# Kernel tuning notes

Measured on AMD Instinct MI355X. Metric: run time of the kernel, lower is better.

Reference implementation:

```python
import jax, jax.numpy as jnp
import numpy as np
from jax import lax

B, C, H, W = 16, 256, 32, 32
DH = 32
HEADS = C // DH          # 8
WSZ = 4                  # window size
K = 4                    # top-k windows
MR = 4                   # mlp_ratio
NWIN = (H // WSZ) * (W // WSZ)  # 64
WS = WSZ * WSZ                  # 16 tokens per window
EPS = 1e-5


def setup_inputs() -> dict:
    key = jax.random.key(0)
    ks = jax.random.split(key, 8)
    w = lambda i, shape: jax.random.normal(ks[i], shape, jnp.float32) * 0.02
    d = {
        'x': jax.random.normal(ks[0], (B, C, H, W), jnp.float32),
        'bn0_g': jax.random.uniform(ks[1], (C,), jnp.float32, 0.5, 1.5),
        'bn0_b': jnp.zeros((C,), jnp.float32),
        'bn0_m': jnp.zeros((C,), jnp.float32),
        'bn0_v': jnp.ones((C,), jnp.float32),
        'w_qkv': w(2, (3 * C, C)),
        'w_merge': w(3, (C, C)),
        'b_merge': jnp.zeros((C,), jnp.float32),
        'w1': w(4, (MR * C, C)),
        'bn1_g': jax.random.uniform(ks[5], (MR * C,), jnp.float32, 0.5, 1.5),
        'bn1_b': jnp.zeros((MR * C,), jnp.float32),
        'bn1_m': jnp.zeros((MR * C,), jnp.float32),
        'bn1_v': jnp.ones((MR * C,), jnp.float32),
        'dw': w(6, (MR * C, 1, 3, 3)),
        'bn2_g': jax.random.uniform(ks[7], (MR * C,), jnp.float32, 0.5, 1.5),
        'bn2_b': jnp.zeros((MR * C,), jnp.float32),
        'bn2_m': jnp.zeros((MR * C,), jnp.float32),
        'bn2_v': jnp.ones((MR * C,), jnp.float32),
        'w2': w(0, (C, MR * C)),
        'bn3_g': jax.random.uniform(ks[1], (C,), jnp.float32, 0.5, 1.5),
        'bn3_b': jnp.zeros((C,), jnp.float32),
        'bn3_m': jnp.zeros((C,), jnp.float32),
        'bn3_v': jnp.ones((C,), jnp.float32),
    }
    return d


def _bn(x, g, b, m, v):
    # eval-mode BatchNorm2d on NCHW
    s = (g / jnp.sqrt(v + EPS))
    return (x - m[None, :, None, None]) * s[None, :, None, None] + b[None, :, None, None]


def _win(t):
    # [B, C, H, W] -> [B, HEADS, NWIN, WS, DH]
    nh, nw = H // WSZ, W // WSZ
    t = t.reshape(B, HEADS, DH, nh, WSZ, nw, WSZ)
    return t.transpose(0, 1, 3, 5, 4, 6, 2).reshape(B, HEADS, NWIN, WS, DH)


def _unwin(t):
    # [B, HEADS, NWIN, WS, DH] -> [B, C, H, W]
    nh, nw = H // WSZ, W // WSZ
    t = t.reshape(B, HEADS, nh, nw, WSZ, WSZ, DH)
    return t.transpose(0, 1, 6, 2, 4, 3, 5).reshape(B, C, H, W)


def _forward(x, bn0_g, bn0_b, bn0_m, bn0_v, w_qkv, w_merge, b_merge,
             w1, bn1_g, bn1_b, bn1_m, bn1_v, dw, bn2_g, bn2_b, bn2_m, bn2_v,
             w2, bn3_g, bn3_b, bn3_m, bn3_v):
    # qkv projection: BN -> GELU -> 1x1 conv (no bias)
    h = jax.nn.gelu(_bn(x, bn0_g, bn0_b, bn0_m, bn0_v), approximate=False)
    qkv = jnp.einsum('oc,bchw->bohw', w_qkv, h)
    q, k, v = jnp.split(qkv, 3, axis=1)

    qw, kw, vw = _win(q), _win(k), _win(v)  # [B,H,NWIN,WS,DH]
    scale = 1.0 / jnp.sqrt(jnp.float32(DH))

    # window-level descriptors -> window-window affinity -> top-k selection
    wsc = jnp.einsum('bhid,bhjd->bhij', qw.mean(3), kw.mean(3)) * scale
    idx = lax.top_k(wsc, K)[1]  # [B,H,NWIN,K]

    # gather top-k kv windows per query window (irregular access)
    gather = jax.vmap(jax.vmap(lambda t, ix: t[ix]))  # over B, HEADS
    kk = gather(kw, idx).reshape(B, HEADS, NWIN, K * WS, DH)
    vv = gather(vw, idx).reshape(B, HEADS, NWIN, K * WS, DH)

    attn = jax.nn.softmax(jnp.einsum('bhnqd,bhnkd->bhnqk', qw, kk) * scale, axis=-1)
    msg = jnp.einsum('bhnqk,bhnkd->bhnqd', attn, vv)
    msg = _unwin(msg)

    # merge (1x1 conv with bias) + residual
    x = x + jnp.einsum('oc,bchw->bohw', w_merge, msg) + b_merge[None, :, None, None]

    # MB mlp: 1x1 expand -> BN -> GELU -> depthwise 3x3 -> BN -> GELU -> 1x1 -> BN
    h = jnp.einsum('oc,bchw->bohw', w1, x)
    h = jax.nn.gelu(_bn(h, bn1_g, bn1_b, bn1_m, bn1_v), approximate=False)
    h = lax.conv_general_dilated(h, dw, (1, 1), 'SAME',
                                 feature_group_count=MR * C,
                                 dimension_numbers=('NCHW', 'OIHW', 'NCHW'))
    h = jax.nn.gelu(_bn(h, bn2_g, bn2_b, bn2_m, bn2_v), approximate=False)
    h = jnp.einsum('oc,bchw->bohw', w2, h)
    h = _bn(h, bn3_g, bn3_b, bn3_m, bn3_v)
    return x + h


def reference(x, bn0_g, bn0_b, bn0_m, bn0_v, w_qkv, w_merge, b_merge,
              w1, bn1_g, bn1_b, bn1_m, bn1_v, dw, bn2_g, bn2_b, bn2_m, bn2_v,
              w2, bn3_g, bn3_b, bn3_m, bn3_v):
    return _forward(x, bn0_g, bn0_b, bn0_m, bn0_v, w_qkv, w_merge, b_merge,
                    w1, bn1_g, bn1_b, bn1_m, bn1_v, dw, bn2_g, bn2_b, bn2_m, bn2_v,
                    w2, bn3_g, bn3_b, bn3_m, bn3_v)
```

## Files before the change

### kernel.cpp

```cpp
#include <hip/hip_runtime.h>
#include <hip/hip_bf16.h>

#define EPSV 1e-5f

typedef short bf16x8 __attribute__((ext_vector_type(8)));
typedef float f32x4 __attribute__((ext_vector_type(4)));

__device__ __forceinline__ float gelu_f(float x) {
    return 0.5f * x * (1.0f + erff(x * 0.70710678118654752f));
}
__device__ __forceinline__ float b2f(unsigned short u) {
    union { float f; unsigned i; } c; c.i = ((unsigned)u) << 16; return c.f;
}
__device__ __forceinline__ unsigned short f2b(float f) {
    __hip_bfloat16 h = __float2bfloat16(f);
    return *reinterpret_cast<unsigned short*>(&h);
}
__device__ __forceinline__ float lo16f(unsigned v) {
    union { float f; unsigned i; } c; c.i = v << 16; return c.f;
}
__device__ __forceinline__ float hi16f(unsigned v) {
    union { float f; unsigned i; } c; c.i = v & 0xffff0000u; return c.f;
}
__device__ __forceinline__ void gload16(const unsigned short* g, unsigned short* l) {
    __builtin_amdgcn_global_load_lds(
        (const __attribute__((address_space(1))) void*)g,
        (__attribute__((address_space(3))) void*)l, 16, 0, 0);
}

__global__ __launch_bounds__(256) void wcvt_k(const float* __restrict__ w,
                                              unsigned short* __restrict__ o, int n4) {
    int i = blockIdx.x * 256 + threadIdx.x;
    if (i >= n4) return;
    float4 v = ((const float4*)w)[i];
    ushort4 u = make_ushort4(f2b(v.x), f2b(v.y), f2b(v.z), f2b(v.w));
    ((ushort4*)o)[i] = u;
}

__global__ __launch_bounds__(256) void wprep_k(const float* __restrict__ wdw,
    const float* __restrict__ g, const float* __restrict__ bt,
    const float* __restrict__ mu, const float* __restrict__ va,
    float* __restrict__ wt, float* __restrict__ scf, float* __restrict__ shf) {
    int ch = blockIdx.x * 256 + threadIdx.x;
    #pragma unroll
    for (int tap = 0; tap < 9; ++tap)
        wt[tap * 1024 + ch] = wdw[ch * 9 + tap];
    float s = g[ch] * rsqrtf(va[ch] + EPSV);
    scf[ch] = s;
    shf[ch] = bt[ch] - mu[ch] * s;
}

__global__ __launch_bounds__(256) void bn0tr_k(const float* __restrict__ x,
    const float* __restrict__ g, const float* __restrict__ bt,
    const float* __restrict__ mu, const float* __restrict__ va,
    unsigned short* __restrict__ h0b, float* __restrict__ xt) {
    __shared__ float tile[64][65];
    int hw0 = blockIdx.x * 64, c0 = blockIdx.y * 64, b = blockIdx.z;
    int t = threadIdx.x;
    int cl = t >> 6, hl = t & 63;
    #pragma unroll
    for (int r = 0; r < 16; ++r)
        tile[r * 4 + cl][hl] = x[((size_t)(b * 256 + c0 + r * 4 + cl)) * 1024 + hw0 + hl];
    __syncthreads();
    int c = c0 + (t & 63);
    float s = g[c] * rsqrtf(va[c] + EPSV);
    float m_ = mu[c], be = bt[c];
    #pragma unroll
    for (int r = 0; r < 16; ++r) {
        int hl2 = r * 4 + (t >> 6);
        float v = tile[t & 63][hl2];
        size_t o = ((size_t)(b * 1024 + hw0 + hl2)) * 256 + c;
        xt[o] = v;
        h0b[o] = f2b(gelu_f((v - m_) * s + be));
    }
}

__global__ __launch_bounds__(256) void hm_k(const float* __restrict__ xt,
    const float* __restrict__ g, const float* __restrict__ bt,
    const float* __restrict__ mu, const float* __restrict__ va,
    float* __restrict__ hm) {
    int blk = blockIdx.x;
    int b = blk >> 6, win = blk & 63;
    int c = threadIdx.x;
    int base = (win >> 3) * 128 + (win & 7) * 4;
    float s = g[c] * rsqrtf(va[c] + EPSV);
    float m_ = mu[c], be = bt[c];
    float acc = 0.f;
    #pragma unroll
    for (int ty = 0; ty < 4; ++ty)
        #pragma unroll
        for (int tx = 0; tx < 4; ++tx) {
            float v = xt[((size_t)(b * 1024 + base + ty * 32 + tx)) * 256 + c];
            acc += gelu_f((v - m_) * s + be);
        }
    hm[(size_t)blk * 256 + c] = acc * (1.f / 16.f);
}

template <int MODE>
__global__ __launch_bounds__(256) void mgemm(
    const unsigned short* __restrict__ A, const unsigned short* __restrict__ X,
    unsigned short* __restrict__ outb, float* __restrict__ outf,
    const float* __restrict__ res,
    const float* __restrict__ p0, const float* __restrict__ p1,
    const float* __restrict__ p2, const float* __restrict__ p3,
    int M, int Kd) {
    __shared__ __align__(16) unsigned short As[4096];
    __shared__ __align__(16) unsigned short Bs[4096];
    const int t = threadIdx.x;
    const int wid = t >> 6, lane = t & 63;
    const int n0 = blockIdx.x * 128, m0 = blockIdx.y * 128, b = blockIdx.z;
    const unsigned short* Ab = A + (size_t)m0 * Kd;
    const unsigned short* Xb = X + ((size_t)b * 1024 + n0) * Kd;

    const int srow = lane >> 2;
    const int skb  = (lane & 3) * 8;
    const int wr = wid >> 1, wc = wid & 1;
    const int lr = lane & 15;
    const int lk = (lane >> 4) * 8;

    f32x4 acc[4][4] = {};

    for (int k0 = 0; k0 < Kd; k0 += 32) {
        #pragma unroll
        for (int i = 0; i < 2; ++i) {
            int chunk = wid * 2 + i;
            int row = chunk * 16 + srow;
            gload16(Ab + (size_t)row * Kd + k0 + skb, &As[chunk * 512]);
            gload16(Xb + (size_t)row * Kd + k0 + skb, &Bs[chunk * 512]);
        }
        __syncthreads();
        bf16x8 af[4], bfv[4];
        #pragma unroll
        for (int mi = 0; mi < 4; ++mi)
            af[mi] = *(const bf16x8*)&As[(wr * 64 + mi * 16 + lr) * 32 + lk];
        #pragma unroll
        for (int ni = 0; ni < 4; ++ni)
            bfv[ni] = *(const bf16x8*)&Bs[(wc * 64 + ni * 16 + lr) * 32 + lk];
        #pragma unroll
        for (int mi = 0; mi < 4; ++mi)
            #pragma unroll
            for (int ni = 0; ni < 4; ++ni)
                acc[mi][ni] = __builtin_amdgcn_mfma_f32_16x16x32_bf16(
                    af[mi], bfv[ni], acc[mi][ni], 0, 0, 0);
        __syncthreads();
    }

    const int crow = (lane >> 4) * 4;
    #pragma unroll
    for (int ni = 0; ni < 4; ++ni) {
        const int n = n0 + wc * 64 + ni * 16 + lr;
        #pragma unroll
        for (int mi = 0; mi < 4; ++mi) {
            const int m = m0 + wr * 64 + mi * 16 + crow;
            f32x4 v = acc[mi][ni];
            size_t o = ((size_t)b * 1024 + n) * (size_t)M + m;
            if (MODE == 0) {
                *(ushort4*)(outb + o) = make_ushort4(f2b(v[0]), f2b(v[1]), f2b(v[2]), f2b(v[3]));
            } else if (MODE == 1) {
                float4 r = *(const float4*)(res + o);
                float4 bi = *(const float4*)(p0 + m);
                float w0 = v[0] + r.x + bi.x, w1 = v[1] + r.y + bi.y;
                float w2 = v[2] + r.z + bi.z, w3 = v[3] + r.w + bi.w;
                *(float4*)(outf + o) = make_float4(w0, w1, w2, w3);
                *(ushort4*)(outb + o) = make_ushort4(f2b(w0), f2b(w1), f2b(w2), f2b(w3));
            } else if (MODE == 2) {
                float4 gg = *(const float4*)(p0 + m);
                float4 be = *(const float4*)(p1 + m);
                float4 mm = *(const float4*)(p2 + m);
                float4 vv = *(const float4*)(p3 + m);
                float h0 = gelu_f((v[0] - mm.x) * (gg.x * rsqrtf(vv.x + EPSV)) + be.x);
                float h1 = gelu_f((v[1] - mm.y) * (gg.y * rsqrtf(vv.y + EPSV)) + be.y);
                float h2 = gelu_f((v[2] - mm.z) * (gg.z * rsqrtf(vv.z + EPSV)) + be.z);
                float h3 = gelu_f((v[3] - mm.w) * (gg.w * rsqrtf(vv.w + EPSV)) + be.w);
                *(ushort4*)(outb + o) = make_ushort4(f2b(h0), f2b(h1), f2b(h2), f2b(h3));
            } else {
                float4 gg = *(const float4*)(p0 + m);
                float4 be = *(const float4*)(p1 + m);
                float4 mm = *(const float4*)(p2 + m);
                float4 vv = *(const float4*)(p3 + m);
                float4 r = *(const float4*)(res + o);
                float y0 = (v[0] - mm.x) * (gg.x * rsqrtf(vv.x + EPSV)) + be.x + r.x;
                float y1 = (v[1] - mm.y) * (gg.y * rsqrtf(vv.y + EPSV)) + be.y + r.y;
                float y2 = (v[2] - mm.z) * (gg.z * rsqrtf(vv.z + EPSV)) + be.z + r.z;
                float y3 = (v[3] - mm.w) * (gg.w * rsqrtf(vv.w + EPSV)) + be.w + r.w;
                *(float4*)(outf + o) = make_float4(y0, y1, y2, y3);
            }
        }
    }
}

__global__ __launch_bounds__(256) void desc2_k(const float* __restrict__ hm,
                                               const float* __restrict__ w_qkv,
                                               float* __restrict__ qkd) {
    __shared__ float As[16][64];
    __shared__ float Bs[16][64];
    float acc[4][4] = {{0.f}};
    const int t = threadIdx.x;
    const int tn = t & 15, tm = t >> 4;
    const int n0 = blockIdx.x * 64;
    const int m0 = blockIdx.y * 64;
    for (int k0 = 0; k0 < 256; k0 += 16) {
        {
            int r  = t >> 2;
            int k4 = (t & 3) << 2;
            float4 a4 = *(const float4*)(w_qkv + (size_t)(m0 + r) * 256 + k0 + k4);
            As[k4 + 0][r] = a4.x; As[k4 + 1][r] = a4.y;
            As[k4 + 2][r] = a4.z; As[k4 + 3][r] = a4.w;
            float4 b4 = *(const float4*)(hm + (size_t)(n0 + r) * 256 + k0 + k4);
            Bs[k4 + 0][r] = b4.x; Bs[k4 + 1][r] = b4.y;
            Bs[k4 + 2][r] = b4.z; Bs[k4 + 3][r] = b4.w;
        }
        __syncthreads();
        #pragma unroll
        for (int kk = 0; kk < 16; ++kk) {
            float4 av = *(const float4*)&As[kk][tm << 2];
            float4 bv = *(const float4*)&Bs[kk][tn << 2];
            float a0[4] = {av.x, av.y, av.z, av.w};
            float b0[4] = {bv.x, bv.y, bv.z, bv.w};
            #pragma unroll
            for (int i = 0; i < 4; ++i)
                #pragma unroll
                for (int j = 0; j < 4; ++j)
                    acc[i][j] += a0[i] * b0[j];
        }
        __syncthreads();
    }
    #pragma unroll
    for (int j = 0; j < 4; ++j) {
        int row = n0 + (tn << 2) + j;
        float4 v = make_float4(acc[0][j], acc[1][j], acc[2][j], acc[3][j]);
        *(float4*)(qkd + (size_t)row * 512 + m0 + (tm << 2)) = v;
    }
}

__global__ __launch_bounds__(256) void aff_k(const float* __restrict__ qkd,
                                             int* __restrict__ idx_out) {
    int bh = blockIdx.x;
    int b = bh >> 3, h = bh & 7;
    __shared__ float qdl[64][33];
    __shared__ float kdl[64][33];
    __shared__ float wsc[64][65];
    int t = threadIdx.x;
    for (int e = t; e < 2048; e += 256) {
        int wn = e >> 5, d = e & 31;
        size_t src = ((size_t)(b * 64 + wn)) * 512 + h * 32 + d;
        qdl[wn][d] = qkd[src];
        kdl[wn][d] = qkd[src + 256];
    }
    __syncthreads();
    {
        int i = t >> 2, j0 = (t & 3) * 16;
        float s[16];
        #pragma unroll
        for (int j = 0; j < 16; ++j) s[j] = 0.f;
        #pragma unroll
        for (int d = 0; d < 32; ++d) {
            float qv = qdl[i][d];
            #pragma unroll
            for (int j = 0; j < 16; ++j) s[j] += qv * kdl[j0 + j][d];
        }
        #pragma unroll
        for (int j = 0; j < 16; ++j) wsc[i][j0 + j] = s[j];
    }
    __syncthreads();
    if (t < 64) {
        float bv[4] = {-1e30f, -1e30f, -1e30f, -1e30f};
        int   bi[4] = {0, 0, 0, 0};
        for (int j = 0; j < 64; ++j) {
            float v = wsc[t][j];
            if (v > bv[3]) {
                int p = 3;
                while (p > 0 && v > bv[p - 1]) {
                    bv[p] = bv[p - 1]; bi[p] = bi[p - 1]; --p;
                }
                bv[p] = v; bi[p] = j;
            }
        }
        int* o = idx_out + (bh * 64 + t) * 4;
        o[0] = bi[0]; o[1] = bi[1]; o[2] = bi[2]; o[3] = bi[3];
    }
}

__global__ __launch_bounds__(256) void attn_k(const unsigned short* __restrict__ qkv,
                                              const int* __restrict__ idx,
                                              unsigned short* __restrict__ msg) {
    int blk = blockIdx.x;
    int win = blk & 63;
    int bh = blk >> 6;
    int b = bh >> 3, h = bh & 7;
    __shared__ float qs[16][32];
    __shared__ float ks[64][32];
    __shared__ float vs[64][32];
    __shared__ float sc[16][64];
    __shared__ int widx[4];
    int t = threadIdx.x;
    if (t < 4) widx[t] = idx[(bh * 64 + win) * 4 + t];
    __syncthreads();
    int qb = (win >> 3) * 128 + (win & 7) * 4;
    for (int e = t; e < 512; e += 256) {
        int tok = e >> 5, d = e & 31;
        int hw = qb + (tok >> 2) * 32 + (tok & 3);
        qs[tok][d] = b2f(qkv[((size_t)(b * 1024 + hw)) * 768 + h * 32 + d]);
    }
    for (int e = t; e < 2048; e += 256) {
        int key = e >> 5, d = e & 31;
        int wsel = widx[key >> 4];
        int tok = key & 15;
        int hw = (wsel >> 3) * 128 + (wsel & 7) * 4 + (tok >> 2) * 32 + (tok & 3);
        size_t base = ((size_t)(b * 1024 + hw)) * 768 + h * 32 + d;
        ks[key][d] = b2f(qkv[base + 256]);
        vs[key][d] = b2f(qkv[base + 512]);
    }
    __syncthreads();
    const float scale = 0.17677669529663688f;
    for (int e = t; e < 1024; e += 256) {
        int r = e >> 6, cidx = e & 63;
        float s = 0.f;
        #pragma unroll
        for (int d = 0; d < 32; ++d) s += qs[r][d] * ks[cidx][d];
        sc[r][cidx] = s * scale;
    }
    __syncthreads();
    {
        int r = t >> 4, c0 = (t & 15) << 2;
        float v0 = sc[r][c0], v1 = sc[r][c0 + 1], v2 = sc[r][c0 + 2], v3 = sc[r][c0 + 3];
        float mx = fmaxf(fmaxf(v0, v1), fmaxf(v2, v3));
        #pragma unroll
        for (int m = 1; m < 16; m <<= 1) mx = fmaxf(mx, __shfl_xor(mx, m));
        float e0 = expf(v0 - mx), e1 = expf(v1 - mx), e2 = expf(v2 - mx), e3 = expf(v3 - mx);
        float sm = e0 + e1 + e2 + e3;
        #pragma unroll
        for (int m = 1; m < 16; m <<= 1) sm += __shfl_xor(sm, m);
        float inv = 1.0f / sm;
        sc[r][c0] = e0 * inv; sc[r][c0 + 1] = e1 * inv;
        sc[r][c0 + 2] = e2 * inv; sc[r][c0 + 3] = e3 * inv;
    }
    __syncthreads();
    for (int e = t; e < 512; e += 256) {
        int tok = e >> 5, d = e & 31;
        float s = 0.f;
        #pragma unroll
        for (int kk = 0; kk < 64; ++kk) s += sc[tok][kk] * vs[kk][d];
        int hw = qb + (tok >> 2) * 32 + (tok & 3);
        msg[((size_t)(b * 1024 + hw)) * 256 + h * 32 + d] = f2b(s);
    }
}

__global__ __launch_bounds__(256) void dw_k(const unsigned short* __restrict__ h1,
    const float* __restrict__ wt, const float* __restrict__ scf,
    const float* __restrict__ shf, unsigned short* __restrict__ h2) {
    int t = threadIdx.x;
    int c8 = t & 127;
    int pl = t >> 7;
    int blk = blockIdx.x;
    int b = blk >> 7;
    int rem = blk & 127;
    int y = rem >> 2;
    int x0 = (rem & 3) * 8;
    int ch0 = c8 * 8;

    float w[9][8];
    #pragma unroll
    for (int tap = 0; tap < 9; ++tap) {
        float4 a = *(const float4*)(wt + tap * 1024 + ch0);
        float4 bq = *(const float4*)(wt + tap * 1024 + ch0 + 4);
        w[tap][0] = a.x; w[tap][1] = a.y; w[tap][2] = a.z; w[tap][3] = a.w;
        w[tap][4] = bq.x; w[tap][5] = bq.y; w[tap][6] = bq.z; w[tap][7] = bq.w;
    }
    float sc[8], sh[8];
    {
        float4 a = *(const float4*)(scf + ch0);
        float4 bq = *(const float4*)(scf + ch0 + 4);
        sc[0]=a.x; sc[1]=a.y; sc[2]=a.z; sc[3]=a.w; sc[4]=bq.x; sc[5]=bq.y; sc[6]=bq.z; sc[7]=bq.w;
        float4 c = *(const float4*)(shf + ch0);
        float4 dq = *(const float4*)(shf + ch0 + 4);
        sh[0]=c.x; sh[1]=c.y; sh[2]=c.z; sh[3]=c.w; sh[4]=dq.x; sh[5]=dq.y; sh[6]=dq.z; sh[7]=dq.w;
    }

    const unsigned short* base = h1 + (size_t)b * 1048576;
    unsigned short* ob = h2 + (size_t)b * 1048576;

    #pragma unroll
    for (int j = 0; j < 4; ++j) {
        int x = x0 + pl + 2 * j;
        float acc[8] = {0.f,0.f,0.f,0.f,0.f,0.f,0.f,0.f};
        #pragma unroll
        for (int dy = -1; dy <= 1; ++dy) {
            int yy = y + dy;
            if (yy < 0 || yy > 31) continue;
            #pragma unroll
            for (int dx = -1; dx <= 1; ++dx) {
                int xx = x + dx;
                if (xx < 0 || xx > 31) continue;
                uint4 u = *(const uint4*)(base + (size_t)(yy * 32 + xx) * 1024 + ch0);
                int tap = (dy + 1) * 3 + (dx + 1);
                acc[0] += lo16f(u.x) * w[tap][0];
                acc[1] += hi16f(u.x) * w[tap][1];
                acc[2] += lo16f(u.y) * w[tap][2];
                acc[3] += hi16f(u.y) * w[tap][3];
                acc[4] += lo16f(u.z) * w[tap][4];
                acc[5] += hi16f(u.z) * w[tap][5];
                acc[6] += lo16f(u.w) * w[tap][6];
                acc[7] += hi16f(u.w) * w[tap][7];
            }
        }
        unsigned short r[8];
        #pragma unroll
        for (int c = 0; c < 8; ++c)
            r[c] = f2b(gelu_f(acc[c] * sc[c] + sh[c]));
        uint4 o;
        o.x = (unsigned)r[0] | ((unsigned)r[1] << 16);
        o.y = (unsigned)r[2] | ((unsigned)r[3] << 16);
        o.z = (unsigned)r[4] | ((unsigned)r[5] << 16);
        o.w = (unsigned)r[6] | ((unsigned)r[7] << 16);
        *(uint4*)(ob + (size_t)(y * 32 + x) * 1024 + ch0) = o;
    }
}

__global__ __launch_bounds__(256) void trout_k(const float* __restrict__ y,
                                               float* __restrict__ out) {
    __shared__ float tile[64][65];
    int hw0 = blockIdx.x * 64, c0 = blockIdx.y * 64, b = blockIdx.z;
    int t = threadIdx.x;
    #pragma unroll
    for (int r = 0; r < 16; ++r) {
        int hl = r * 4 + (t >> 6);
        tile[t & 63][hl] = y[((size_t)(b * 1024 + hw0 + hl)) * 256 + c0 + (t & 63)];
    }
    __syncthreads();
    #pragma unroll
    for (int r = 0; r < 16; ++r) {
        int cl = r * 4 + (t >> 6);
        out[((size_t)(b * 256 + c0 + cl)) * 1024 + hw0 + (t & 63)] = tile[cl][t & 63];
    }
}

extern "C" void kernel_launch(void* const* d_in, const int* in_sizes, int n_in,
                              void* d_out, int out_size, void* d_ws, size_t ws_size,
                              hipStream_t stream) {
    const float* x      = (const float*)d_in[0];
    const float* bn0_g  = (const float*)d_in[1];
    const float* bn0_b  = (const float*)d_in[2];
    const float* bn0_m  = (const float*)d_in[3];
    const float* bn0_v  = (const float*)d_in[4];
    const float* w_qkv  = (const float*)d_in[5];
    const float* w_merge= (const float*)d_in[6];
    const float* b_merge= (const float*)d_in[7];
    const float* w1     = (const float*)d_in[8];
    const float* bn1_g  = (const float*)d_in[9];
    const float* bn1_b  = (const float*)d_in[10];
    const float* bn1_m  = (const float*)d_in[11];
    const float* bn1_v  = (const float*)d_in[12];
    const float* dw     = (const float*)d_in[13];
    const float* bn2_g  = (const float*)d_in[14];
    const float* bn2_b  = (const float*)d_in[15];
    const float* bn2_m  = (const float*)d_in[16];
    const float* bn2_v  = (const float*)d_in[17];
    const float* w2     = (const float*)d_in[18];
    const float* bn3_g  = (const float*)d_in[19];
    const float* bn3_b  = (const float*)d_in[20];
    const float* bn3_m  = (const float*)d_in[21];
    const float* bn3_v  = (const float*)d_in[22];
    float* out = (float*)d_out;

    char* w = (char*)d_ws;
    unsigned short* h0b   = (unsigned short*)(w);
    unsigned short* qkvb  = (unsigned short*)(w + 8388608);
    unsigned short* msgb  = (unsigned short*)(w + 33554432);
    unsigned short* xrb   = (unsigned short*)(w + 41943040);
    unsigned short* h1b   = (unsigned short*)(w + 50331648);
    unsigned short* h2b   = (unsigned short*)(w + 83886080);
    float*  xt    = (float*)(w + 117440512);
    float*  xrf   = (float*)(w + 134217728);
    float*  yf    = (float*)(w + 150994944);
    float*  hm    = (float*)(w + 167772160);
    unsigned short* wqkvb = (unsigned short*)(w + 168820736);
    unsigned short* wmrgb = (unsigned short*)(w + 169213952);
    unsigned short* w1b   = (unsigned short*)(w + 169345024);
    unsigned short* w2b   = (unsigned short*)(w + 169869312);
    int*    idx   = (int*)(w + 170393600);
    float*  wtbuf = (float*)(w + 170524672);
    float*  scbuf = (float*)(w + 170561536);
    float*  shbuf = (float*)(w + 170565632);
    float*  qkdbuf= (float*)(w + 170569728);

    wcvt_k<<<192, 256, 0, stream>>>(w_qkv, wqkvb, 49152);
    wcvt_k<<<64,  256, 0, stream>>>(w_merge, wmrgb, 16384);
    wcvt_k<<<256, 256, 0, stream>>>(w1, w1b, 65536);
    wcvt_k<<<256, 256, 0, stream>>>(w2, w2b, 65536);
    wprep_k<<<4, 256, 0, stream>>>(dw, bn2_g, bn2_b, bn2_m, bn2_v, wtbuf, scbuf, shbuf);

    bn0tr_k<<<dim3(16, 4, 16), 256, 0, stream>>>(x, bn0_g, bn0_b, bn0_m, bn0_v, h0b, xt);
    hm_k<<<1024, 256, 0, stream>>>(xt, bn0_g, bn0_b, bn0_m, bn0_v, hm);
    mgemm<0><<<dim3(8, 6, 16), 256, 0, stream>>>(wqkvb, h0b, qkvb, nullptr,
        nullptr, nullptr, nullptr, nullptr, nullptr, 768, 256);
    desc2_k<<<dim3(16, 8), 256, 0, stream>>>(hm, w_qkv, qkdbuf);
    aff_k<<<128, 256, 0, stream>>>(qkdbuf, idx);
    attn_k<<<8192, 256, 0, stream>>>(qkvb, idx, msgb);
    mgemm<1><<<dim3(8, 2, 16), 256, 0, stream>>>(wmrgb, msgb, xrb, xrf,
        xt, b_merge, nullptr, nullptr, nullptr, 256, 256);
    mgemm<2><<<dim3(8, 8, 16), 256, 0, stream>>>(w1b, xrb, h1b, nullptr,
        nullptr, bn1_g, bn1_b, bn1_m, bn1_v, 1024, 256);
    dw_k<<<2048, 256, 0, stream>>>(h1b, wtbuf, scbuf, shbuf, h2b);
    mgemm<3><<<dim3(8, 2, 16), 256, 0, stream>>>(w2b, h2b, nullptr, yf,
        xrf, bn3_g, bn3_b, bn3_m, bn3_v, 256, 1024);
    trout_k<<<dim3(16, 4, 16), 256, 0, stream>>>(yf, out);
}
```

Measured before the change: 377.7 us.

## Rewrite windowed attention with per-wave MFMA tiles and bf16 shared memory

The attention kernel now handles one (batch, head, window) per wavefront, packing four into each block, and launches a quarter as many blocks. QK^T and PV are computed with 16x16x32 bf16 MFMA instructions instead of scalar fp32 dot products. Q, K and V are staged in shared memory as bf16 using vectorized 8-byte loads, with V stored transposed. Softmax runs directly on the MFMA accumulators. The aim is to remove the scalar-FMA and shared-memory bandwidth cost, at the price of rounding probabilities to bf16 and doing scattered 2-byte writes for the transposed V.

```diff
diff --git a/kernel.cpp b/kernel.cpp
--- a/kernel.cpp
+++ b/kernel.cpp
@@ -284,65 +284,92 @@
 __global__ __launch_bounds__(256) void attn_k(const unsigned short* __restrict__ qkv,
                                               const int* __restrict__ idx,
                                               unsigned short* __restrict__ msg) {
-    int blk = blockIdx.x;
-    int win = blk & 63;
-    int bh = blk >> 6;
-    int b = bh >> 3, h = bh & 7;
-    __shared__ float qs[16][32];
-    __shared__ float ks[64][32];
-    __shared__ float vs[64][32];
-    __shared__ float sc[16][64];
-    __shared__ int widx[4];
-    int t = threadIdx.x;
-    if (t < 4) widx[t] = idx[(bh * 64 + win) * 4 + t];
-    __syncthreads();
-    int qb = (win >> 3) * 128 + (win & 7) * 4;
-    for (int e = t; e < 512; e += 256) {
-        int tok = e >> 5, d = e & 31;
+    __shared__ __align__(16) unsigned short qs[4][16][40];
+    __shared__ __align__(16) unsigned short ks[4][64][40];
+    __shared__ __align__(16) unsigned short vt[4][32][72];
+    __shared__ __align__(16) unsigned short ps[4][16][72];
+    const int t = threadIdx.x;
+    const int wid = t >> 6, lane = t & 63;
+    const int g = blockIdx.x * 4 + wid;
+    const int win = g & 63;
+    const int bh = g >> 6;
+    const int b = bh >> 3, h = bh & 7;
+    const int qb = (win >> 3) * 128 + (win & 7) * 4;
+    const int* widx = idx + (bh * 64 + win) * 4;
+
+    for (int e = lane; e < 128; e += 64) {
+        int tok = e >> 3, d4 = (e & 7) * 4;
         int hw = qb + (tok >> 2) * 32 + (tok & 3);
-        qs[tok][d] = b2f(qkv[((size_t)(b * 1024 + hw)) * 768 + h * 32 + d]);
-    }
-    for (int e = t; e < 2048; e += 256) {
-        int key = e >> 5, d = e & 31;
+        uint2 u = *(const uint2*)&qkv[((size_t)(b * 1024 + hw)) * 768 + h * 32 + d4];
+        *(uint2*)&qs[wid][tok][d4] = u;
+    }
+    for (int e = lane; e < 512; e += 64) {
+        int key = e >> 3, d4 = (e & 7) * 4;
         int wsel = widx[key >> 4];
         int tok = key & 15;
         int hw = (wsel >> 3) * 128 + (wsel & 7) * 4 + (tok >> 2) * 32 + (tok & 3);
-        size_t base = ((size_t)(b * 1024 + hw)) * 768 + h * 32 + d;
-        ks[key][d] = b2f(qkv[base + 256]);
-        vs[key][d] = b2f(qkv[base + 512]);
+        size_t base = ((size_t)(b * 1024 + hw)) * 768 + h * 32 + d4;
+        uint2 uk = *(const uint2*)&qkv[base + 256];
+        uint2 uv = *(const uint2*)&qkv[base + 512];
+        *(uint2*)&ks[wid][key][d4] = uk;
+        vt[wid][d4 + 0][key] = (unsigned short)(uv.x & 0xffffu);
+        vt[wid][d4 + 1][key] = (unsigned short)(uv.x >> 16);
+        vt[wid][d4 + 2][key] = (unsigned short)(uv.y & 0xffffu);
+        vt[wid][d4 + 3][key] = (unsigned short)(uv.y >> 16);
     }
     __syncthreads();
+
+    const int lr = lane & 15;
+    const int lk8 = (lane >> 4) * 8;
     const float scale = 0.17677669529663688f;
-    for (int e = t; e < 1024; e += 256) {
-        int r = e >> 6, cidx = e & 63;
-        float s = 0.f;
-        #pragma unroll
-        for (int d = 0; d < 32; ++d) s += qs[r][d] * ks[cidx][d];
-        sc[r][cidx] = s * scale;
-    }
-    __syncthreads();
-    {
-        int r = t >> 4, c0 = (t & 15) << 2;
-        float v0 = sc[r][c0], v1 = sc[r][c0 + 1], v2 = sc[r][c0 + 2], v3 = sc[r][c0 + 3];
-        float mx = fmaxf(fmaxf(v0, v1), fmaxf(v2, v3));
+    f32x4 zero = {0.f, 0.f, 0.f, 0.f};
+
+    bf16x8 qA = *(const bf16x8*)&qs[wid][lr][lk8];
+    f32x4 sa[4];
+    #pragma unroll
+    for (int kt = 0; kt < 4; ++kt) {
+        bf16x8 kB = *(const bf16x8*)&ks[wid][kt * 16 + lr][lk8];
+        sa[kt] = __builtin_amdgcn_mfma_f32_16x16x32_bf16(qA, kB, zero, 0, 0, 0);
+    }
+    #pragma unroll
+    for (int i = 0; i < 4; ++i) {
+        float s0 = sa[0][i] * scale, s1 = sa[1][i] * scale;
+        float s2 = sa[2][i] * scale, s3 = sa[3][i] * scale;
+        float mx = fmaxf(fmaxf(s0, s1), fmaxf(s2, s3));
         #pragma unroll
         for (int m = 1; m < 16; m <<= 1) mx = fmaxf(mx, __shfl_xor(mx, m));
-        float e0 = expf(v0 - mx), e1 = expf(v1 - mx), e2 = expf(v2 - mx), e3 = expf(v3 - mx);
+        float e0 = expf(s0 - mx), e1 = expf(s1 - mx);
+        float e2 = expf(s2 - mx), e3 = expf(s3 - mx);
         float sm = e0 + e1 + e2 + e3;
         #pragma unroll
         for (int m = 1; m < 16; m <<= 1) sm += __shfl_xor(sm, m);
         float inv = 1.0f / sm;
-        sc[r][c0] = e0 * inv; sc[r][c0 + 1] = e1 * inv;
-        sc[r][c0 + 2] = e2 * inv; sc[r][c0 + 3] = e3 * inv;
+        int row = (lane >> 4) * 4 + i;
+        ps[wid][row][ 0 + lr] = f2b(e0 * inv);
+        ps[wid][row][16 + lr] = f2b(e1 * inv);
+        ps[wid][row][32 + lr] = f2b(e2 * inv);
+        ps[wid][row][48 + lr] = f2b(e3 * inv);
     }
     __syncthreads();
-    for (int e = t; e < 512; e += 256) {
-        int tok = e >> 5, d = e & 31;
-        float s = 0.f;
-        #pragma unroll
-        for (int kk = 0; kk < 64; ++kk) s += sc[tok][kk] * vs[kk][d];
-        int hw = qb + (tok >> 2) * 32 + (tok & 3);
-        msg[((size_t)(b * 1024 + hw)) * 256 + h * 32 + d] = f2b(s);
+    f32x4 oa[2] = {zero, zero};
+    #pragma unroll
+    for (int kh = 0; kh < 2; ++kh) {
+        bf16x8 pA = *(const bf16x8*)&ps[wid][lr][kh * 32 + lk8];
+        #pragma unroll
+        for (int nt = 0; nt < 2; ++nt) {
+            bf16x8 vB = *(const bf16x8*)&vt[wid][nt * 16 + lr][kh * 32 + lk8];
+            oa[nt] = __builtin_amdgcn_mfma_f32_16x16x32_bf16(pA, vB, oa[nt], 0, 0, 0);
+        }
+    }
+    #pragma unroll
+    for (int nt = 0; nt < 2; ++nt) {
+        int d = nt * 16 + lr;
+        #pragma unroll
+        for (int i = 0; i < 4; ++i) {
+            int tok = (lane >> 4) * 4 + i;
+            int hw = qb + (tok >> 2) * 32 + (tok & 3);
+            msg[((size_t)(b * 1024 + hw)) * 256 + h * 32 + d] = f2b(oa[nt][i]);
+        }
     }
 }
 
@@ -496,7 +523,7 @@
         nullptr, nullptr, nullptr, nullptr, nullptr, 768, 256);
     desc2_k<<<dim3(16, 8), 256, 0, stream>>>(hm, w_qkv, qkdbuf);
     aff_k<<<128, 256, 0, stream>>>(qkdbuf, idx);
-    attn_k<<<8192, 256, 0, stream>>>(qkvb, idx, msgb);
+    attn_k<<<2048, 256, 0, stream>>>(qkvb, idx, msgb);
     mgemm<1><<<dim3(8, 2, 16), 256, 0, stream>>>(wmrgb, msgb, xrb, xrf,
         xt, b_merge, nullptr, nullptr, nullptr, 256, 256);
     mgemm<2><<<dim3(8, 8, 16), 256, 0, stream>>>(w1b, xrb, h1b, nullptr,
```

Result: faster. 345.2 us (-8.6%).
